# Kernel tuning notes

Measured on AMD Instinct MI355X. Metric: run time of the kernel, lower is better.

Reference implementation:

```python
import jax, jax.numpy as jnp
import numpy as np

B, S, DIM = 2, 2048, 2048
N_HEADS, N_KV_HEADS, HEAD_DIM = 16, 4, 128
ROPE_THETA = 10000.0
N_REP = N_HEADS // N_KV_HEADS


def make_freq_cis(seq_len, head_dim, theta):
    # (seq_len, head_dim//2, 2, 2) rotation matrices [[cos,-sin],[sin,cos]]
    freqs = 1.0 / (theta ** (np.arange(0, head_dim, 2, dtype=np.float32) / head_dim))
    t = np.arange(seq_len, dtype=np.float32)
    ang = np.outer(t, freqs)  # [S, head_dim//2]
    cos, sin = np.cos(ang), np.sin(ang)
    row0 = np.stack([cos, -sin], axis=-1)
    row1 = np.stack([sin, cos], axis=-1)
    return jnp.asarray(np.stack([row0, row1], axis=-2))  # [S, hd/2, 2, 2]


def setup_inputs() -> dict:
    key = jax.random.key(0)
    ks = jax.random.split(key, 5)
    std = DIM ** -0.5
    x = jax.random.normal(ks[0], (B, S, DIM), dtype=jnp.float32)
    wq = jax.random.normal(ks[1], (N_HEADS * HEAD_DIM, DIM), dtype=jnp.float32) * std
    wk = jax.random.normal(ks[2], (N_KV_HEADS * HEAD_DIM, DIM), dtype=jnp.float32) * std
    wv = jax.random.normal(ks[3], (N_KV_HEADS * HEAD_DIM, DIM), dtype=jnp.float32) * std
    wo = jax.random.normal(ks[4], (DIM, N_HEADS * HEAD_DIM), dtype=jnp.float32) * std
    freq_cis = make_freq_cis(S, HEAD_DIM, ROPE_THETA)
    return {"x": x, "freq_cis": freq_cis, "wq": wq, "wk": wk, "wv": wv, "wo": wo}


def apply_rotary(xh, fc):
    # xh: [B,S,H,hd]; fc: [S, hd/2, 2, 2]
    b, s, h, hd = xh.shape
    xr = xh.reshape(b, s, h, hd // 2, 2)
    out = jnp.einsum('bshdj,sdij->bshdi', xr, fc)
    return out.reshape(b, s, h, hd)


def attention_fwd(x, freq_cis, wq, wk, wv, wo):
    b, s, _ = x.shape
    xq = (x @ wq.T).reshape(b, s, N_HEADS, HEAD_DIM)
    xk = (x @ wk.T).reshape(b, s, N_KV_HEADS, HEAD_DIM)
    xv = (x @ wv.T).reshape(b, s, N_KV_HEADS, HEAD_DIM)
    xq = apply_rotary(xq, freq_cis[:s])
    xk = apply_rotary(xk, freq_cis[:s])
    # GQA repeat_kv (repeat_interleave along head dim)
    xk = jnp.repeat(xk, N_REP, axis=2)
    xv = jnp.repeat(xv, N_REP, axis=2)
    scale = HEAD_DIM ** -0.5
    scores = jnp.einsum('bqhd,bkhd->bhqk', xq, xk) * scale
    causal = jnp.tril(jnp.ones((s, s), dtype=bool))
    scores = jnp.where(causal[None, None], scores, jnp.float32(-1e30))
    probs = jax.nn.softmax(scores, axis=-1)
    out = jnp.einsum('bhqk,bkhd->bqhd', probs, xv).reshape(b, s, N_HEADS * HEAD_DIM)
    return out @ wo.T


def reference(x, freq_cis, wq, wk, wv, wo):
    return attention_fwd(x, freq_cis, wq, wk, wv, wo)
```

## Files before the change

### kernel.cpp

```cpp
#include <hip/hip_runtime.h>

#define S_LEN 2048
#define N_B 2
#define N_H 16
#define N_KVH 4
#define HD 128
#define LDQ 2048
#define LDK 1024

typedef __bf16 bf16x8 __attribute__((ext_vector_type(8)));
typedef float f32x4 __attribute__((ext_vector_type(4)));
typedef float f32x16 __attribute__((ext_vector_type(16)));
typedef int v2i __attribute__((ext_vector_type(2)));

__device__ __forceinline__ float bf2f(unsigned short u){
  unsigned int x = ((unsigned int)u) << 16; float f;
  __builtin_memcpy(&f, &x, 4); return f;
}
__device__ __forceinline__ unsigned short f2bf(float f){
  unsigned int x; __builtin_memcpy(&x, &f, 4);
  unsigned int r = x + 0x7fff + ((x >> 16) & 1);
  return (unsigned short)(r >> 16);
}
__device__ __forceinline__ unsigned int cvt_pk_bf16(float lo, float hi){
  unsigned int u;
  asm("v_cvt_pk_bf16_f32 %0, %1, %2" : "=v"(u) : "v"(lo), "v"(hi));
  return u;
}
__device__ __forceinline__ void gload16(const void* g, void* l){
  __builtin_amdgcn_global_load_lds((const __attribute__((address_space(1))) void*)g,
                                   (__attribute__((address_space(3))) void*)l, 16, 0, 0);
}

__global__ void cast_bf16(const float* __restrict__ in, unsigned short* __restrict__ out, int n8){
  int i = blockIdx.x * 256 + threadIdx.x;
  if (i >= n8) return;
  const float4* p = (const float4*)in + (size_t)i * 2;
  float4 a = p[0], b = p[1];
  uint4 o;
  o.x = (unsigned)f2bf(a.x) | ((unsigned)f2bf(a.y) << 16);
  o.y = (unsigned)f2bf(a.z) | ((unsigned)f2bf(a.w) << 16);
  o.z = (unsigned)f2bf(b.x) | ((unsigned)f2bf(b.y) << 16);
  o.w = (unsigned)f2bf(b.z) | ((unsigned)f2bf(b.w) << 16);
  ((uint4*)out)[i] = o;
}

__global__ void rope_kernel(unsigned short* __restrict__ X, const float* __restrict__ FC,
                            int cpr_log2, int ld_log2, int n8){
  int i = blockIdx.x * 256 + threadIdx.x;
  if (i >= n8) return;
  int row = i >> cpr_log2;
  int col = (i & ((1 << cpr_log2) - 1)) << 3;
  size_t idx = ((size_t)row << ld_log2) + col;
  int s = row & (S_LEN - 1);
  int d = col & (HD - 1);
  uint4 v = *(const uint4*)(X + idx);
  unsigned short* pv = (unsigned short*)&v;
  const float4* f4 = (const float4*)FC + ((size_t)s * 64 + (d >> 1));
  uint4 ov; unsigned short* po = (unsigned short*)&ov;
#pragma unroll
  for (int p = 0; p < 4; p++){
    float4 f = f4[p];
    float e = bf2f(pv[2*p]), o = bf2f(pv[2*p+1]);
    po[2*p]   = f2bf(f.x * e + f.y * o);
    po[2*p+1] = f2bf(f.z * e + f.w * o);
  }
  *(uint4*)(X + idx) = ov;
}

__global__ void transpose_v(const unsigned short* __restrict__ V, unsigned short* __restrict__ Vt, int ld){
  __shared__ unsigned short tile[32][33];
  int t = threadIdx.x;
  int s0 = blockIdx.x * 32;
  int c0 = blockIdx.y * 32;
  int r = t >> 3, cg = (t & 7) * 4;
  uint2 in2 = *(const uint2*)(V + (size_t)(s0 + r) * ld + c0 + cg);
  unsigned short* pi = (unsigned short*)&in2;
  tile[r][cg+0] = pi[0]; tile[r][cg+1] = pi[1]; tile[r][cg+2] = pi[2]; tile[r][cg+3] = pi[3];
  __syncthreads();
  int b = s0 >> 11, sl = s0 & (S_LEN - 1);
  int kvh = c0 >> 7, dd0 = c0 & (HD - 1);
  int dd = t >> 3, sg = (t & 7) * 4;
  uint2 o2; unsigned short* po = (unsigned short*)&o2;
  po[0] = tile[sg+0][dd]; po[1] = tile[sg+1][dd]; po[2] = tile[sg+2][dd]; po[3] = tile[sg+3][dd];
  *(uint2*)(Vt + (size_t)((b * N_KVH + kvh) * HD + dd0 + dd) * S_LEN + sl + sg) = o2;
}

__device__ __forceinline__ void storeC(float* C, size_t idx, float v){ C[idx] = v; }
__device__ __forceinline__ void storeC(unsigned short* C, size_t idx, float v){ C[idx] = f2bf(v); }

template <typename OutT>
__global__ __launch_bounds__(256, 2) void gemm_nt(const unsigned short* __restrict__ A,
                                                  const unsigned short* __restrict__ Bm,
                                                  OutT* __restrict__ C,
                                                  int M, int N, int K, int nbn){
  extern __shared__ char smem[];
  char* sA = smem; char* sB = smem + 16384;
  int bid = blockIdx.x;
  bid = (bid & 7) * (gridDim.x >> 3) + (bid >> 3);
  int bn = bid % nbn, bm = bid / nbn;
  int row0 = bm * 128, col0 = bn * 128;
  int t = threadIdx.x; int w = t >> 6, l = t & 63;
  int lr = l & 15, lg = l >> 4;
  int srow = t >> 3;
  int sg = (t & 7) ^ (srow & 7);
  const unsigned short* agp = A + (size_t)(row0 + srow) * K + sg * 8;
  const unsigned short* bgp = Bm + (size_t)(col0 + srow) * K + sg * 8;
  int wr = w >> 1, wc = w & 1;
  f32x4 acc[4][4] = {};
  for (int k0 = 0; k0 < K; k0 += 64){
    __syncthreads();
#pragma unroll
    for (int i = 0; i < 4; i++){
      gload16(agp + (size_t)i * 32 * K + k0, sA + i * 4096 + w * 1024);
      gload16(bgp + (size_t)i * 32 * K + k0, sB + i * 4096 + w * 1024);
    }
    __syncthreads();
#pragma unroll
    for (int kk = 0; kk < 2; kk++){
      bf16x8 af[4], bfv[4];
#pragma unroll
      for (int m = 0; m < 4; m++){
        int row = wr * 64 + m * 16 + lr;
        int kg = kk * 4 + lg;
        af[m] = *(const bf16x8*)(sA + row * 128 + ((kg ^ (row & 7)) << 4));
      }
#pragma unroll
      for (int n = 0; n < 4; n++){
        int row = wc * 64 + n * 16 + lr;
        int kg = kk * 4 + lg;
        bfv[n] = *(const bf16x8*)(sB + row * 128 + ((kg ^ (row & 7)) << 4));
      }
#pragma unroll
      for (int m = 0; m < 4; m++)
#pragma unroll
        for (int n = 0; n < 4; n++)
          acc[m][n] = __builtin_amdgcn_mfma_f32_16x16x32_bf16(af[m], bfv[n], acc[m][n], 0, 0, 0);
    }
  }
#pragma unroll
  for (int m = 0; m < 4; m++)
#pragma unroll
    for (int n = 0; n < 4; n++)
#pragma unroll
      for (int r = 0; r < 4; r++){
        int rr = row0 + wr * 64 + m * 16 + lg * 4 + r;
        int cc = col0 + wc * 64 + n * 16 + lr;
        storeC(C, (size_t)rr * N + cc, acc[m][n][r]);
      }
}

template <typename OutT>
__global__ __launch_bounds__(512, 2) void gemm_tpl(const unsigned short* __restrict__ A,
                                                   const unsigned short* __restrict__ Bm,
                                                   OutT* __restrict__ C,
                                                   int M, int N, int K, int nbn){
  extern __shared__ char smem[];
  int bid = blockIdx.x;
  bid = (bid & 7) * (gridDim.x >> 3) + (bid >> 3);
  int bn = bid % nbn, bm = bid / nbn;
  int row0 = bm * 128, col0 = bn * 256;
  int t = threadIdx.x, w = t >> 6, l = t & 63;
  int lr = l & 15, lg = l >> 4;
  int wm = w >> 2, wn = w & 3;
  int srow = t >> 3;
  int sg = (t & 7) ^ (srow & 7);
  const unsigned short* agp = A + (size_t)(row0 + srow) * K + sg * 8;
  const unsigned short* bgp = Bm + (size_t)(col0 + srow) * K + sg * 8;
  int nk = K >> 6;
  f32x4 acc[4][4] = {};

#define TPL_STAGE(j, s) do {                                                   \
    char* base_ = smem + (s) * 49152;                                          \
    int k0_ = (j) << 6;                                                        \
    _Pragma("unroll")                                                          \
    for (int i_ = 0; i_ < 2; i_++)                                             \
      gload16(agp + (size_t)i_ * 64 * K + k0_, base_ + i_ * 8192 + w * 1024);  \
    _Pragma("unroll")                                                          \
    for (int i_ = 0; i_ < 4; i_++)                                             \
      gload16(bgp + (size_t)i_ * 64 * K + k0_, base_ + 16384 + i_ * 8192 + w * 1024); \
  } while(0)

  TPL_STAGE(0, 0);
  TPL_STAGE(1, 1);
  int slot = 0;
  for (int j = 0; j < nk; j++){
    if (j + 1 < nk) asm volatile("s_waitcnt vmcnt(6)" ::: "memory");
    else            asm volatile("s_waitcnt vmcnt(0)" ::: "memory");
    __builtin_amdgcn_s_barrier();
    asm volatile("" ::: "memory");
    char* sA = smem + slot * 49152;
    char* sB = sA + 16384;
    bf16x8 af[2][4], bf[2][4];
#pragma unroll
    for (int kk = 0; kk < 2; kk++){
#pragma unroll
      for (int m = 0; m < 4; m++){
        int row = wm * 64 + m * 16 + lr;
        int kg = kk * 4 + lg;
        af[kk][m] = *(const bf16x8*)(sA + row * 128 + ((kg ^ (row & 7)) << 4));
      }
#pragma unroll
      for (int n = 0; n < 4; n++){
        int row = wn * 64 + n * 16 + lr;
        int kg = kk * 4 + lg;
        bf[kk][n] = *(const bf16x8*)(sB + row * 128 + ((kg ^ (row & 7)) << 4));
      }
    }
    if (j + 2 < nk){
      int sn = slot + 2; if (sn >= 3) sn -= 3;
      TPL_STAGE(j + 2, sn);
    }
    __builtin_amdgcn_s_setprio(1);
#pragma unroll
    for (int kk = 0; kk < 2; kk++)
#pragma unroll
      for (int m = 0; m < 4; m++)
#pragma unroll
        for (int n = 0; n < 4; n++)
          acc[m][n] = __builtin_amdgcn_mfma_f32_16x16x32_bf16(af[kk][m], bf[kk][n], acc[m][n], 0, 0, 0);
    __builtin_amdgcn_s_setprio(0);
    slot++; if (slot == 3) slot = 0;
  }
#undef TPL_STAGE
#pragma unroll
  for (int m = 0; m < 4; m++)
#pragma unroll
    for (int n = 0; n < 4; n++)
#pragma unroll
      for (int r = 0; r < 4; r++){
        int rr = row0 + wm * 64 + m * 16 + lg * 4 + r;
        int cc = col0 + wn * 64 + n * 16 + lr;
        storeC(C, (size_t)rr * N + cc, acc[m][n][r]);
      }
}

__global__ __launch_bounds__(256, 2) void attn_fwd(const unsigned short* __restrict__ Q,
                                                   const unsigned short* __restrict__ Kb,
                                                   const unsigned short* __restrict__ Vt,
                                                   unsigned short* __restrict__ P0,
                                                   unsigned short* __restrict__ P1,
                                                   float2* __restrict__ ML){
  extern __shared__ char smem[];
  const float SOFT_C = 0.088388347648318447f * 1.4426950408889634f;
  const float THR_RAW = 62.0f;
  int bid = blockIdx.x;
  bid = ((bid & 7) << 6) | (bid >> 3);
  int slot = bid & 15, h = (bid >> 4) & 15, b = bid >> 8;
  int p = slot & 7, half = slot >> 3;
  int kvh = h >> 2;
  int t = threadIdx.x, w = t >> 6, l = t & 63;
  int lq = l & 31, lh = l >> 5;
  unsigned short* Pout = half ? P1 : P0;
  float2* mlb = ML + half * (N_B * S_LEN * N_H);

  int gA = (t & 15) ^ (t >> 4);
  const unsigned short* kgp = Kb + ((size_t)(b * S_LEN) + (t >> 4)) * LDK + kvh * HD + gA * 8;
  int gV = (t & 7) ^ ((t >> 3) & 7);
  const unsigned short* vgp = Vt + ((size_t)((b * N_KVH + kvh) * HD) + (t >> 3)) * S_LEN + gV * 8;

  for (int phase = 0; phase < 2; phase++){
    int qt = phase ? (15 - p) : p;
    int q_lane = qt * 128 + w * 32 + lq;
    const unsigned short* qbase = Q + ((size_t)(b * S_LEN + q_lane)) * LDQ + h * HD + lh * 8;
    bf16x8 qf[8];
#pragma unroll
    for (int ks = 0; ks < 8; ks++)
      qf[ks] = *(const bf16x8*)(qbase + ks * 16);

    f32x16 o_acc[4] = {};
    float m_run = -1e4f, l_run = 0.f;
    int t_begin = half ? (qt + 1) : 0;
    int t_end   = half ? (2 * qt + 2) : (qt + 1);

    int pk0 = t_begin * 64;
#pragma unroll
    for (int m = 0; m < 4; m++)
      gload16(kgp + (size_t)(pk0 + m * 16) * LDK, smem + m * 4096 + w * 1024);
#pragma unroll
    for (int i = 0; i < 4; i++)
      gload16(vgp + (size_t)i * 32 * S_LEN + pk0, smem + 16384 + i * 4096 + w * 1024);
    __syncthreads();

    int cur = 0;
    for (int tix = t_begin; tix < t_end; tix++){
      int k0 = tix * 64;
      char* sK = smem + (cur << 15);
      char* sV = sK + 16384;
      if (tix + 1 < t_end){
        char* nb = smem + ((cur ^ 1) << 15);
        int nk0 = k0 + 64;
#pragma unroll
        for (int m = 0; m < 4; m++)
          gload16(kgp + (size_t)(nk0 + m * 16) * LDK, nb + m * 4096 + w * 1024);
#pragma unroll
        for (int i = 0; i < 4; i++)
          gload16(vgp + (size_t)i * 32 * S_LEN + nk0, nb + 16384 + i * 4096 + w * 1024);
      }

      f32x16 sc[2] = {};
      __builtin_amdgcn_s_setprio(1);
#pragma unroll
      for (int ks = 0; ks < 8; ks++){
#pragma unroll
        for (int n = 0; n < 2; n++){
          int row = n * 32 + lq;
          int pg = (ks * 2 + lh) ^ (row & 15);
          bf16x8 kf = *(const bf16x8*)(sK + row * 256 + pg * 16);
          sc[n] = __builtin_amdgcn_mfma_f32_32x32x16_bf16(kf, qf[ks], sc[n], 0, 0, 0);
        }
      }
      __builtin_amdgcn_s_setprio(0);
      if (tix >= 2 * qt){
#pragma unroll
        for (int n = 0; n < 2; n++)
#pragma unroll
          for (int reg = 0; reg < 16; reg++){
            int kv = k0 + n * 32 + (reg & 3) + 8 * (reg >> 2) + 4 * lh;
            if (kv > q_lane) sc[n][reg] = -1e30f;
          }
      }
      float tmax = sc[0][0];
#pragma unroll
      for (int n = 0; n < 2; n++)
#pragma unroll
        for (int reg = 0; reg < 16; reg++) tmax = fmaxf(tmax, sc[n][reg]);
      tmax = fmaxf(tmax, __shfl_xor(tmax, 32));
      if (!__all(tmax - m_run <= THR_RAW)){
        float nm = fmaxf(m_run, tmax);
        float rs = exp2f((m_run - nm) * SOFT_C);
        m_run = nm;
        l_run *= rs;
#pragma unroll
        for (int n = 0; n < 4; n++)
#pragma unroll
          for (int j = 0; j < 16; j++) o_acc[n][j] *= rs;
      }
      float lsum = 0.f;
#pragma unroll
      for (int n = 0; n < 2; n++)
#pragma unroll
        for (int reg = 0; reg < 16; reg++){
          float pv = exp2f((sc[n][reg] - m_run) * SOFT_C);
          sc[n][reg] = pv;
          lsum += pv;
        }
      lsum += __shfl_xor(lsum, 32);
      l_run += lsum;

      bf16x8 pb[4];
#pragma unroll
      for (int ks = 0; ks < 4; ks++){
        int n = ks >> 1;
        int R0 = (2 * ks) & 3, R1 = (2 * ks + 1) & 3;
        unsigned int WA0 = cvt_pk_bf16(sc[n][4 * R0 + 0], sc[n][4 * R0 + 1]);
        unsigned int WA1 = cvt_pk_bf16(sc[n][4 * R0 + 2], sc[n][4 * R0 + 3]);
        unsigned int WB0 = cvt_pk_bf16(sc[n][4 * R1 + 0], sc[n][4 * R1 + 1]);
        unsigned int WB1 = cvt_pk_bf16(sc[n][4 * R1 + 2], sc[n][4 * R1 + 3]);
        v2i s0 = __builtin_amdgcn_permlane32_swap((int)WA0, (int)WB0, false, false);
        v2i s1 = __builtin_amdgcn_permlane32_swap((int)WA1, (int)WB1, false, false);
        unsigned int pu[4] = {(unsigned int)s0.x, (unsigned int)s1.x,
                              (unsigned int)s0.y, (unsigned int)s1.y};
        pb[ks] = *(bf16x8*)pu;
      }
      __builtin_amdgcn_s_setprio(1);
#pragma unroll
      for (int n = 0; n < 4; n++){
#pragma unroll
        for (int ks = 0; ks < 4; ks++){
          int row = n * 32 + lq;
          int pg = (ks * 2 + lh) ^ (row & 7);
          bf16x8 vf = *(const bf16x8*)(sV + row * 128 + pg * 16);
          o_acc[n] = __builtin_amdgcn_mfma_f32_32x32x16_bf16(vf, pb[ks], o_acc[n], 0, 0, 0);
        }
      }
      __builtin_amdgcn_s_setprio(0);
      __syncthreads();
      cur ^= 1;
    }
    unsigned short* ob = Pout + ((size_t)(b * S_LEN + q_lane)) * LDQ + h * HD + 4 * lh;
#pragma unroll
    for (int n = 0; n < 4; n++)
#pragma unroll
      for (int g = 0; g < 4; g++){
        unsigned int u0 = cvt_pk_bf16(o_acc[n][4 * g + 0], o_acc[n][4 * g + 1]);
        unsigned int u1 = cvt_pk_bf16(o_acc[n][4 * g + 2], o_acc[n][4 * g + 3]);
        uint2 o2; o2.x = u0; o2.y = u1;
        *(uint2*)(ob + n * 32 + g * 8) = o2;
      }
    if (lh == 0)
      mlb[(size_t)(b * S_LEN + q_lane) * N_H + h] = make_float2(m_run, l_run);
  }
}

__global__ void attn_merge(unsigned short* __restrict__ P0, const unsigned short* __restrict__ P1,
                           const float2* __restrict__ ML){
  const float SOFT_C = 0.088388347648318447f * 1.4426950408889634f;
  int tid = blockIdx.x * 256 + threadIdx.x;
  float2 a = ML[tid >> 4];
  float2 c = ML[(N_B * S_LEN * N_H) + (tid >> 4)];
  float m = fmaxf(a.x, c.x);
  float w0 = exp2f((a.x - m) * SOFT_C) * a.y;
  float w1 = exp2f((c.x - m) * SOFT_C) * c.y;
  float inv = 1.0f / (w0 + w1);
  float s0 = exp2f((a.x - m) * SOFT_C) * inv;
  float s1 = exp2f((c.x - m) * SOFT_C) * inv;
  uint4 u0 = *(const uint4*)(P0 + (size_t)tid * 8);
  uint4 u1 = *(const uint4*)(P1 + (size_t)tid * 8);
  unsigned short* q0 = (unsigned short*)&u0;
  unsigned short* q1 = (unsigned short*)&u1;
  uint4 o;
  unsigned int* po = (unsigned int*)&o;
#pragma unroll
  for (int j = 0; j < 4; j++){
    float lo = s0 * bf2f(q0[2*j])   + s1 * bf2f(q1[2*j]);
    float hi = s0 * bf2f(q0[2*j+1]) + s1 * bf2f(q1[2*j+1]);
    po[j] = cvt_pk_bf16(lo, hi);
  }
  *(uint4*)(P0 + (size_t)tid * 8) = o;
}

extern "C" void kernel_launch(void* const* d_in, const int* in_sizes, int n_in,
                              void* d_out, int out_size, void* d_ws, size_t ws_size,
                              hipStream_t stream) {
  const float* x  = (const float*)d_in[0];
  const float* fc = (const float*)d_in[1];
  const float* wq = (const float*)d_in[2];
  const float* wk = (const float*)d_in[3];
  const float* wv = (const float*)d_in[4];
  const float* wo = (const float*)d_in[5];
  float* out = (float*)d_out;

  char* ws = (char*)d_ws;
  unsigned short* xb  = (unsigned short*)(ws);
  unsigned short* wqb = (unsigned short*)(ws + 16777216);
  unsigned short* wkb = (unsigned short*)(ws + 25165824);
  unsigned short* wvb = (unsigned short*)(ws + 27262976);
  unsigned short* wob = (unsigned short*)(ws + 29360128);
  unsigned short* qb_ = (unsigned short*)(ws + 37748736);
  unsigned short* kvb = (unsigned short*)(ws + 54525952);
  unsigned short* vtb = (unsigned short*)(ws + 62914560);
  unsigned short* ab_ = (unsigned short*)(ws + 67108864);
  unsigned short* p1_ = xb;
  float2*         ml_ = (float2*)wqb;

  cast_bf16<<<4096, 256, 0, stream>>>(x,  xb,  1048576);
  cast_bf16<<<2048, 256, 0, stream>>>(wq, wqb, 524288);
  cast_bf16<<<512,  256, 0, stream>>>(wk, wkb, 131072);
  cast_bf16<<<512,  256, 0, stream>>>(wv, wvb, 131072);
  cast_bf16<<<2048, 256, 0, stream>>>(wo, wob, 524288);

  gemm_tpl<unsigned short><<<256, 512, 147456, stream>>>(xb, wqb, qb_, 4096, 2048, 2048, 8);
  gemm_nt<unsigned short><<<256, 256, 32768, stream>>>(xb, wkb, kvb, 4096, 1024, 2048, 8);

  rope_kernel<<<4096, 256, 0, stream>>>(qb_, fc, 8, 11, 1048576);
  rope_kernel<<<1024, 256, 0, stream>>>(kvb, fc, 6, 10, 262144);

  transpose_v<<<dim3(128, 16), 256, 0, stream>>>(kvb + 512, vtb, 1024);

  attn_fwd<<<512, 256, 65536, stream>>>(qb_, kvb, vtb, ab_, p1_, ml_);
  attn_merge<<<4096, 256, 0, stream>>>(ab_, p1_, ml_);

  gemm_tpl<float><<<256, 512, 147456, stream>>>(ab_, wob, out, 4096, 2048, 2048, 8);
}
```

Before: 213.5 us.

## Fuse cast kernels, split GEMM k-step into halves, restage attention K/V layout

New measurement: 216.4 us. Within noise of the previous version (+1.3%).

```diff
diff --git a/kernel.cpp b/kernel.cpp
--- a/kernel.cpp
+++ b/kernel.cpp
@@ -32,17 +32,26 @@
                                    (__attribute__((address_space(3))) void*)l, 16, 0, 0);
 }
 
-__global__ void cast_bf16(const float* __restrict__ in, unsigned short* __restrict__ out, int n8){
+__global__ void cast_all(const float* __restrict__ x,  const float* __restrict__ wq,
+                         const float* __restrict__ wk, const float* __restrict__ wv,
+                         const float* __restrict__ wo, unsigned short* __restrict__ xb,
+                         unsigned short* __restrict__ wqb, unsigned short* __restrict__ wkb,
+                         unsigned short* __restrict__ wvb, unsigned short* __restrict__ wob){
   int i = blockIdx.x * 256 + threadIdx.x;
-  if (i >= n8) return;
-  const float4* p = (const float4*)in + (size_t)i * 2;
+  const float* in; unsigned short* out; int j;
+  if (i < 1048576)      { in = x;  out = xb;  j = i; }
+  else if (i < 1572864) { in = wq; out = wqb; j = i - 1048576; }
+  else if (i < 1703936) { in = wk; out = wkb; j = i - 1572864; }
+  else if (i < 1835008) { in = wv; out = wvb; j = i - 1703936; }
+  else                  { in = wo; out = wob; j = i - 1835008; }
+  const float4* p = (const float4*)in + (size_t)j * 2;
   float4 a = p[0], b = p[1];
   uint4 o;
   o.x = (unsigned)f2bf(a.x) | ((unsigned)f2bf(a.y) << 16);
   o.y = (unsigned)f2bf(a.z) | ((unsigned)f2bf(a.w) << 16);
   o.z = (unsigned)f2bf(b.x) | ((unsigned)f2bf(b.y) << 16);
   o.w = (unsigned)f2bf(b.z) | ((unsigned)f2bf(b.w) << 16);
-  ((uint4*)out)[i] = o;
+  ((uint4*)out)[j] = o;
 }
 
 __global__ void rope_kernel(unsigned short* __restrict__ X, const float* __restrict__ FC,
@@ -170,19 +179,24 @@
   int nk = K >> 6;
   f32x4 acc[4][4] = {};
 
-#define TPL_STAGE(j, s) do {                                                   \
+#define TPL_STAGE_H1(j, s) do {                                                \
     char* base_ = smem + (s) * 49152;                                          \
     int k0_ = (j) << 6;                                                        \
     _Pragma("unroll")                                                          \
     for (int i_ = 0; i_ < 2; i_++)                                             \
       gload16(agp + (size_t)i_ * 64 * K + k0_, base_ + i_ * 8192 + w * 1024);  \
+    gload16(bgp + k0_, base_ + 16384 + w * 1024);                              \
+  } while(0)
+#define TPL_STAGE_H2(j, s) do {                                                \
+    char* base_ = smem + (s) * 49152;                                          \
+    int k0_ = (j) << 6;                                                        \
     _Pragma("unroll")                                                          \
-    for (int i_ = 0; i_ < 4; i_++)                                             \
+    for (int i_ = 1; i_ < 4; i_++)                                             \
       gload16(bgp + (size_t)i_ * 64 * K + k0_, base_ + 16384 + i_ * 8192 + w * 1024); \
   } while(0)
 
-  TPL_STAGE(0, 0);
-  TPL_STAGE(1, 1);
+  TPL_STAGE_H1(0, 0); TPL_STAGE_H2(0, 0);
+  TPL_STAGE_H1(1, 1); TPL_STAGE_H2(1, 1);
   int slot = 0;
   for (int j = 0; j < nk; j++){
     if (j + 1 < nk) asm volatile("s_waitcnt vmcnt(6)" ::: "memory");
@@ -191,38 +205,58 @@
     asm volatile("" ::: "memory");
     char* sA = smem + slot * 49152;
     char* sB = sA + 16384;
-    bf16x8 af[2][4], bf[2][4];
-#pragma unroll
-    for (int kk = 0; kk < 2; kk++){
+    int sn = slot + 2; if (sn >= 3) sn -= 3;
+    {
+      bf16x8 af[4], bfv[4];
 #pragma unroll
       for (int m = 0; m < 4; m++){
         int row = wm * 64 + m * 16 + lr;
-        int kg = kk * 4 + lg;
-        af[kk][m] = *(const bf16x8*)(sA + row * 128 + ((kg ^ (row & 7)) << 4));
+        af[m] = *(const bf16x8*)(sA + row * 128 + ((lg ^ (row & 7)) << 4));
       }
 #pragma unroll
       for (int n = 0; n < 4; n++){
         int row = wn * 64 + n * 16 + lr;
-        int kg = kk * 4 + lg;
-        bf[kk][n] = *(const bf16x8*)(sB + row * 128 + ((kg ^ (row & 7)) << 4));
-      }
-    }
-    if (j + 2 < nk){
-      int sn = slot + 2; if (sn >= 3) sn -= 3;
-      TPL_STAGE(j + 2, sn);
-    }
-    __builtin_amdgcn_s_setprio(1);
-#pragma unroll
-    for (int kk = 0; kk < 2; kk++)
+        bfv[n] = *(const bf16x8*)(sB + row * 128 + ((lg ^ (row & 7)) << 4));
+      }
+      if (j + 2 < nk) TPL_STAGE_H1(j + 2, sn);
+      __builtin_amdgcn_s_barrier();
+      __builtin_amdgcn_s_setprio(1);
 #pragma unroll
       for (int m = 0; m < 4; m++)
 #pragma unroll
         for (int n = 0; n < 4; n++)
-          acc[m][n] = __builtin_amdgcn_mfma_f32_16x16x32_bf16(af[kk][m], bf[kk][n], acc[m][n], 0, 0, 0);
-    __builtin_amdgcn_s_setprio(0);
+          acc[m][n] = __builtin_amdgcn_mfma_f32_16x16x32_bf16(af[m], bfv[n], acc[m][n], 0, 0, 0);
+      __builtin_amdgcn_s_setprio(0);
+      __builtin_amdgcn_s_barrier();
+    }
+    {
+      bf16x8 af[4], bfv[4];
+#pragma unroll
+      for (int m = 0; m < 4; m++){
+        int row = wm * 64 + m * 16 + lr;
+        int kg = 4 + lg;
+        af[m] = *(const bf16x8*)(sA + row * 128 + ((kg ^ (row & 7)) << 4));
+      }
+#pragma unroll
+      for (int n = 0; n < 4; n++){
+        int row = wn * 64 + n * 16 + lr;
+        int kg = 4 + lg;
+        bfv[n] = *(const bf16x8*)(sB + row * 128 + ((kg ^ (row & 7)) << 4));
+      }
+      if (j + 2 < nk) TPL_STAGE_H2(j + 2, sn);
+      __builtin_amdgcn_s_barrier();
+      __builtin_amdgcn_s_setprio(1);
+#pragma unroll
+      for (int m = 0; m < 4; m++)
+#pragma unroll
+        for (int n = 0; n < 4; n++)
+          acc[m][n] = __builtin_amdgcn_mfma_f32_16x16x32_bf16(af[m], bfv[n], acc[m][n], 0, 0, 0);
+      __builtin_amdgcn_s_setprio(0);
+    }
     slot++; if (slot == 3) slot = 0;
   }
-#undef TPL_STAGE
+#undef TPL_STAGE_H1
+#undef TPL_STAGE_H2
 #pragma unroll
   for (int m = 0; m < 4; m++)
 #pragma unroll
@@ -254,10 +288,8 @@
   unsigned short* Pout = half ? P1 : P0;
   float2* mlb = ML + half * (N_B * S_LEN * N_H);
 
-  int gA = (t & 15) ^ (t >> 4);
-  const unsigned short* kgp = Kb + ((size_t)(b * S_LEN) + (t >> 4)) * LDK + kvh * HD + gA * 8;
-  int gV = (t & 7) ^ ((t >> 3) & 7);
-  const unsigned short* vgp = Vt + ((size_t)((b * N_KVH + kvh) * HD) + (t >> 3)) * S_LEN + gV * 8;
+  const unsigned short* kgp = Kb + ((size_t)(b * S_LEN) + (t & 63)) * LDK + kvh * HD + (t >> 6) * 8;
+  const unsigned short* vgp = Vt + ((size_t)((b * N_KVH + kvh) * HD) + (t & 127)) * S_LEN + (t >> 7) * 8;
 
   for (int phase = 0; phase < 2; phase++){
     int qt = phase ? (15 - p) : p;
@@ -273,29 +305,28 @@
     int t_begin = half ? (qt + 1) : 0;
     int t_end   = half ? (2 * qt + 2) : (qt + 1);
 
-    int pk0 = t_begin * 64;
-#pragma unroll
-    for (int m = 0; m < 4; m++)
-      gload16(kgp + (size_t)(pk0 + m * 16) * LDK, smem + m * 4096 + w * 1024);
-#pragma unroll
-    for (int i = 0; i < 4; i++)
-      gload16(vgp + (size_t)i * 32 * S_LEN + pk0, smem + 16384 + i * 4096 + w * 1024);
+    {
+      int k0 = t_begin * 64;
+#pragma unroll
+      for (int i = 0; i < 4; i++){
+        gload16(kgp + (size_t)k0 * LDK + i * 32, smem + i * 4096 + t * 16);
+        gload16(vgp + k0 + i * 16, smem + 16384 + i * 4096 + t * 16);
+      }
+    }
     __syncthreads();
 
     int cur = 0;
     for (int tix = t_begin; tix < t_end; tix++){
       int k0 = tix * 64;
-      char* sK = smem + (cur << 15);
-      char* sV = sK + 16384;
+      char* kb = smem + (cur << 15);
       if (tix + 1 < t_end){
         char* nb = smem + ((cur ^ 1) << 15);
         int nk0 = k0 + 64;
 #pragma unroll
-        for (int m = 0; m < 4; m++)
-          gload16(kgp + (size_t)(nk0 + m * 16) * LDK, nb + m * 4096 + w * 1024);
-#pragma unroll
-        for (int i = 0; i < 4; i++)
-          gload16(vgp + (size_t)i * 32 * S_LEN + nk0, nb + 16384 + i * 4096 + w * 1024);
+        for (int i = 0; i < 4; i++){
+          gload16(kgp + (size_t)nk0 * LDK + i * 32, nb + i * 4096 + t * 16);
+          gload16(vgp + nk0 + i * 16, nb + 16384 + i * 4096 + t * 16);
+        }
       }
 
       f32x16 sc[2] = {};
@@ -304,9 +335,7 @@
       for (int ks = 0; ks < 8; ks++){
 #pragma unroll
         for (int n = 0; n < 2; n++){
-          int row = n * 32 + lq;
-          int pg = (ks * 2 + lh) ^ (row & 15);
-          bf16x8 kf = *(const bf16x8*)(sK + row * 256 + pg * 16);
+          bf16x8 kf = *(const bf16x8*)(kb + (ks * 2 + lh) * 1024 + n * 512 + lq * 16);
           sc[n] = __builtin_amdgcn_mfma_f32_32x32x16_bf16(kf, qf[ks], sc[n], 0, 0, 0);
         }
       }
@@ -368,9 +397,7 @@
       for (int n = 0; n < 4; n++){
 #pragma unroll
         for (int ks = 0; ks < 4; ks++){
-          int row = n * 32 + lq;
-          int pg = (ks * 2 + lh) ^ (row & 7);
-          bf16x8 vf = *(const bf16x8*)(sV + row * 128 + pg * 16);
+          bf16x8 vf = *(const bf16x8*)(kb + 16384 + (ks * 2 + lh) * 2048 + n * 512 + lq * 16);
           o_acc[n] = __builtin_amdgcn_mfma_f32_32x32x16_bf16(vf, pb[ks], o_acc[n], 0, 0, 0);
         }
       }
@@ -444,11 +471,7 @@
   unsigned short* p1_ = xb;
   float2*         ml_ = (float2*)wqb;
 
-  cast_bf16<<<4096, 256, 0, stream>>>(x,  xb,  1048576);
-  cast_bf16<<<2048, 256, 0, stream>>>(wq, wqb, 524288);
-  cast_bf16<<<512,  256, 0, stream>>>(wk, wkb, 131072);
-  cast_bf16<<<512,  256, 0, stream>>>(wv, wvb, 131072);
-  cast_bf16<<<2048, 256, 0, stream>>>(wo, wob, 524288);
+  cast_all<<<9216, 256, 0, stream>>>(x, wq, wk, wv, wo, xb, wqb, wkb, wvb, wob);
 
   gemm_tpl<unsigned short><<<256, 512, 147456, stream>>>(xb, wqb, qb_, 4096, 2048, 2048, 8);
   gemm_nt<unsigned short><<<256, 256, 32768, stream>>>(xb, wkb, kvb, 4096, 1024, 2048, 8);
```
